# Optimization experiments

Measured on AMD Instinct MI355X. Metric: run time of the kernel, lower is better.

## Reference

```python
import jax, jax.numpy as jnp
import numpy as np

EPS = 1e-5
CLIP = 1.0

@jax.custom_vjp
def ste_sign(x):
    return jnp.sign(x)

def _ste_fwd(x):
    return jnp.sign(x), x

def _ste_bwd(x, g):
    return (g * (jnp.abs(x) <= CLIP).astype(g.dtype),)

ste_sign.defvjp(_ste_fwd, _ste_bwd)

def conv2d(x, w, stride, pad):
    return jax.lax.conv_general_dilated(
        x, w, window_strides=(stride, stride), padding=[(pad, pad), (pad, pad)],
        dimension_numbers=('NCHW', 'OIHW', 'NCHW'))

def bn(x, g, b, m, v):
    inv = g / jnp.sqrt(v + EPS)
    return x * inv[None, :, None, None] + (b - m * inv)[None, :, None, None]

def setup_inputs() -> dict:
    key = jax.random.key(0)
    ks = jax.random.split(key, 16)
    def rn(k, shape, scale=0.05):
        return jax.random.normal(k, shape, dtype=jnp.float32) * scale
    C = [64, 128, 128, 192, 192]
    d = {}
    d['x'] = jax.random.normal(ks[0], (128, 1, 128, 128), dtype=jnp.float32)
    d['conv1_w'] = rn(ks[1], (C[0], 1, 3, 3), 0.3)
    d['conv1_b'] = rn(ks[2], (C[0],))
    d['w2'] = rn(ks[3], (C[1], C[0], 3, 3), 0.3)
    d['w3'] = rn(ks[4], (C[2], C[1], 3, 3), 0.3)
    d['w4'] = rn(ks[5], (C[3], C[2], 3, 3), 0.3)
    d['w5'] = rn(ks[6], (C[4], C[3], 1, 1), 0.3)
    d['conv6_w'] = rn(ks[7], (12, C[4], 1, 1), 0.1)
    d['conv6_b'] = rn(ks[8], (12,))
    d['fc_w'] = rn(ks[9], (12, 12), 0.2)
    d['fc_b'] = rn(ks[10], (12,))
    for i, c in enumerate(C):
        kk = jax.random.split(jax.random.fold_in(key, 100 + i), 4)
        d[f'bn{i+1}_g'] = 1.0 + rn(kk[0], (c,), 0.1)
        d[f'bn{i+1}_b'] = rn(kk[1], (c,), 0.1)
        d[f'bn{i+1}_m'] = rn(kk[2], (c,), 0.1)
        d[f'bn{i+1}_v'] = 1.0 + jnp.abs(rn(kk[3], (c,), 0.1))
    return d

def reference(x, conv1_w, conv1_b, w2, w3, w4, w5, conv6_w, conv6_b, fc_w, fc_b,
              bn1_g, bn1_b, bn1_m, bn1_v, bn2_g, bn2_b, bn2_m, bn2_v,
              bn3_g, bn3_b, bn3_m, bn3_v, bn4_g, bn4_b, bn4_m, bn4_v,
              bn5_g, bn5_b, bn5_m, bn5_v):
    # conv1 (float) + BN + ReLU
    h = conv2d(x, conv1_w, 2, 1) + conv1_b[None, :, None, None]
    h = jax.nn.relu(bn(h, bn1_g, bn1_b, bn1_m, bn1_v))
    # binarized conv blocks: sign(activation) conv sign(weight)
    h = conv2d(ste_sign(h), ste_sign(w2), 1, 1)
    h = jax.nn.relu(bn(h, bn2_g, bn2_b, bn2_m, bn2_v))
    h = conv2d(ste_sign(h), ste_sign(w3), 2, 1)
    h = jax.nn.relu(bn(h, bn3_g, bn3_b, bn3_m, bn3_v))
    h = conv2d(ste_sign(h), ste_sign(w4), 1, 1)
    h = jax.nn.relu(bn(h, bn4_g, bn4_b, bn4_m, bn4_v))
    h = conv2d(ste_sign(h), ste_sign(w5), 1, 0)
    h = jax.nn.relu(bn(h, bn5_g, bn5_b, bn5_m, bn5_v))
    # 1x1 conv to classes, global average pool, FC, softmax
    h = conv2d(h, conv6_w, 1, 0) + conv6_b[None, :, None, None]
    h = jnp.mean(h, axis=(2, 3))  # [B, num_classes]
    logits = h @ fc_w.T + fc_b
    return jax.nn.softmax(logits, axis=1)
```

## Files before the change

kernel.cpp:

```cpp
#include <hip/hip_runtime.h>
#include <cstdint>

using u64 = unsigned long long;
using u32 = unsigned int;
typedef __attribute__((ext_vector_type(4))) int int4v;
typedef __attribute__((ext_vector_type(16))) int int16v;

struct PrepArgs {
  const float* bng[5]; const float* bnb[5]; const float* bnm[5]; const float* bnv[5];
  float* inv1; float* cc1; float* inv5; float* cc5;
  int* thr[3]; int* flp[3];
  const float* w[4];
  u64* wp[4]; u64* wz[4];
  u32* flags;
};

__global__ __launch_bounds__(256) void prep_all(PrepArgs a) {
  int i = blockIdx.x * 256 + threadIdx.x;
  if (i < 704) {
    const int off[6] = {0, 64, 192, 320, 512, 704};
    int l = 0;
    while (i >= off[l + 1]) ++l;
    int c = i - off[l];
    float iv = __fdiv_rn(a.bng[l][c], __fsqrt_rn(__fadd_rn(a.bnv[l][c], 1e-5f)));
    float cb = __fsub_rn(a.bnb[l][c], __fmul_rn(a.bnm[l][c], iv));
    if (l == 0) { a.inv1[c] = iv; a.cc1[c] = cb; }
    else if (l == 4) { a.inv5[c] = iv; a.cc5[c] = cb; }
    else {
      auto pred = [&](int v_) {
        return __fadd_rn(__fmul_rn((float)v_, iv), cb) > 0.f;
      };
      int Tx, fl;
      if (iv == 0.f) { Tx = pred(0) ? -100000 : 100000; fl = 0; }
      else if (iv > 0.f) {
        if (pred(-2048)) { Tx = -100000; fl = 0; }
        else if (!pred(2048)) { Tx = 100000; fl = 0; }
        else {
          int lo = -2048, hi = 2048;
          while (hi - lo > 1) { int md = (lo + hi) >> 1; if (pred(md)) hi = md; else lo = md; }
          Tx = hi; fl = 0;
        }
      } else {
        if (pred(2048)) { Tx = -100000; fl = -1; }
        else if (!pred(-2048)) { Tx = 100000; fl = -1; }
        else {
          int lo = -2048, hi = 2048;
          while (hi - lo > 1) { int md = (lo + hi) >> 1; if (pred(md)) lo = md; else hi = md; }
          Tx = lo ^ -1; fl = -1;
        }
      }
      a.thr[l - 1][c] = Tx; a.flp[l - 1][c] = fl;
    }
    return;
  }
  int j = i - 704;
  if (j >= 7488) return;
  const int poff[5] = {0, 1152, 3456, 6912, 7488};
  const int ICt[4] = {64, 128, 128, 192};
  const int Kt[4]  = {9, 9, 9, 1};
  const int Wt[4]  = {1, 2, 2, 3};
  int l = 0;
  while (j >= poff[l + 1]) ++l;
  int idx = j - poff[l];
  int W = Wt[l], K = Kt[l], IC = ICt[l];
  int wi = idx % W;
  int rest = idx / W;
  int t = rest % K;
  int oc = rest / K;
  u64 p = 0, z = 0;
  int icbase = wi * 64;
  int nb = IC - icbase; if (nb > 64) nb = 64;
  const float* w = a.w[l];
  for (int b = 0; b < nb; ++b) {
    float f = w[((size_t)oc * IC + (icbase + b)) * K + t];
    if (f > 0.f) p |= (1ull << b);
    else if (f == 0.f) z |= (1ull << b);
  }
  a.wp[l][idx] = p;
  a.wz[l][idx] = z;
  if (z) atomicOr(a.flags + l, 1u);
}

template <int CINW, int COUT>
__global__ __launch_bounds__(256) void prep_bfrag(const float* __restrict__ w,
                                                  signed char* __restrict__ bf) {
  constexpr int NKC = 9 * CINW;
  constexpr int NT = COUT / 16;
  constexpr int CIN = 64 * CINW;
  int idx = blockIdx.x * 256 + threadIdx.x;
  if (idx >= NT * NKC * 64) return;
  int lane = idx & 63;
  int rest = idx >> 6;
  int kc = rest % NKC;
  int t = rest / NKC;
  int tap = kc / CINW, wd = kc % CINW;
  int n = t * 16 + (lane & 15);
  int icb = wd * 64 + (lane >> 4) * 16;
  signed char* dst = bf + (size_t)idx * 16;
#pragma unroll
  for (int i = 0; i < 16; ++i) {
    float f = w[((size_t)n * CIN + icb + i) * 9 + tap];
    dst[i] = (f > 0.f) ? 1 : ((f < 0.f) ? -1 : 0);
  }
}

__global__ __launch_bounds__(256) void prep_bfrag32(const float* __restrict__ w,
                                                    signed char* __restrict__ bf) {
  int idx = blockIdx.x * 256 + threadIdx.x;
  if (idx >= 4 * 18 * 64) return;
  int lane = idx & 63;
  int rest = idx >> 6;
  int s = rest % 18;
  int t = rest / 18;
  int oc = t * 32 + (lane & 31);
  int kbase = s * 32 + (lane >> 5) * 16;
  signed char* dst = bf + (size_t)idx * 16;
#pragma unroll
  for (int i = 0; i < 16; ++i) {
    int k = kbase + i;
    int ch = k & 63, tap = k >> 6;
    float f = w[((size_t)oc * 64 + ch) * 9 + tap];
    dst[i] = (f > 0.f) ? 1 : ((f < 0.f) ? -1 : 0);
  }
}

__global__ __launch_bounds__(256) void pad_x(const float* __restrict__ x,
                                             float* __restrict__ xpad) {
  int idx = blockIdx.x * 256 + threadIdx.x;
  int c = idx & 127, r = (idx >> 7) & 127, n = idx >> 14;
  xpad[((size_t)n * 130 + r + 1) * 136 + c + 1] = x[idx];
}

__global__ __launch_bounds__(256) void conv1_bin(
    const float* __restrict__ xpad, const float* __restrict__ w1, const float* __restrict__ b1,
    const float* __restrict__ inv1, const float* __restrict__ cc1,
    u64* __restrict__ a1p) {
  int tid = threadIdx.x, lane = tid & 63;
  int rb = __builtin_amdgcn_readfirstlane(tid >> 6);
  int blk = blockIdx.x;
  int y = (blk % 16) * 4 + rb;
  int n = blk / 16;
  float W[9];
#pragma unroll
  for (int t = 0; t < 9; ++t) W[t] = w1[lane * 9 + t];
  float bias = b1[lane], iv = inv1[lane], cb = cc1[lane];
  const float* sb = xpad + ((size_t)n * 130 + 2 * y) * 136;
  float A[12], B[12], C[12];
  u64 rowm = 0;
  int xb = 0;

#define FLD(BUF, POFF)                                     \
  _Pragma("unroll") for (int _r = 0; _r < 3; ++_r)         \
  _Pragma("unroll") for (int _j = 0; _j < 4; ++_j)         \
    BUF[_r * 4 + _j] = sb[_r * 136 + (POFF) + _j];
#define FPX(XO, B0F, C0, B1F, C1, B2F, C2) {                          \
  float acc = 0.f;                                                    \
  _Pragma("unroll") for (int _r = 0; _r < 3; ++_r)                    \
    acc += B0F[_r * 4 + (C0)] * W[_r * 3 + 0]                         \
         + B1F[_r * 4 + (C1)] * W[_r * 3 + 1]                         \
         + B2F[_r * 4 + (C2)] * W[_r * 3 + 2];                        \
  float h = __fadd_rn(acc, bias);                                     \
  float bnv = __fadd_rn(__fmul_rn(h, iv), cb);                        \
  u64 _m = __ballot(bnv > 0.f);                                       \
  rowm = (lane == (XO)) ? _m : rowm; }
#define FSTEP(BA, BB, BC, POFF, XB)  \
  FLD(BC, (POFF) + 8);               \
  FPX((XB), BA, 0, BA, 1, BA, 2);    \
  FPX((XB) + 1, BA, 2, BA, 3, BB, 0);

  FLD(A, 0); FLD(B, 4);
  for (int g = 0; g < 10; ++g) {
    FSTEP(A, B, C, 0, xb);
    FSTEP(B, C, A, 4, xb + 2);
    FSTEP(C, A, B, 8, xb + 4);
    sb += 12; xb += 6;
  }
  FSTEP(A, B, C, 0, xb);
  FSTEP(B, C, A, 4, xb + 2);
  a1p[((size_t)n * 66 + (y + 1)) * 68 + lane + 1] = rowm;
#undef FLD
#undef FPX
#undef FSTEP
}

__global__ __launch_bounds__(256, 2) void bconv2_32(
    const u64* __restrict__ ain, const signed char* __restrict__ bf,
    const int* __restrict__ thr, const int* __restrict__ flp,
    u64* __restrict__ aout) {
  __shared__ int4v bs[4 * 18 * 64];
  int tid = threadIdx.x, lane = tid & 63;
  int wv = __builtin_amdgcn_readfirstlane(tid >> 6);
  int pos = blockIdx.x * 4 + wv;
  int xg = pos & 1;
  int y = (pos >> 1) & 63;
  int n = pos >> 7;
  int ln31 = lane & 31;
  int kg16 = (lane >> 5) * 16;
  int px = xg * 32 + ln31;

  const int4v* bfv = (const int4v*)bf;
  int4v breg[18];
#pragma unroll
  for (int i = 0; i < 18; ++i) breg[i] = bfv[tid + i * 256];

  const u64* abase = ain + ((size_t)n * 66 + y) * 68 + px;
  int4v af[18];
#pragma unroll
  for (int tap = 0; tap < 9; ++tap) {
    int dy = tap / 3, dx = tap % 3;
    u64 aw = abase[(size_t)dy * 68 + dx];
#pragma unroll
    for (int h = 0; h < 2; ++h) {
      u32 t16 = (u32)(aw >> (h * 32 + kg16)) & 0xFFFFu;
      int4v v;
      v.x = (int)((((t16      ) & 0xFu) * 0x00204081u) & 0x01010101u);
      v.y = (int)((((t16 >> 4 ) & 0xFu) * 0x00204081u) & 0x01010101u);
      v.z = (int)((((t16 >> 8 ) & 0xFu) * 0x00204081u) & 0x01010101u);
      v.w = (int)((((t16 >> 12) & 0xFu) * 0x00204081u) & 0x01010101u);
      af[tap * 2 + h] = v;
    }
  }

  int txv[4], flv[4];
#pragma unroll
  for (int t = 0; t < 4; ++t) { txv[t] = thr[t * 32 + ln31]; flv[t] = flp[t * 32 + ln31]; }

#pragma unroll
  for (int i = 0; i < 18; ++i) bs[tid + i * 256] = breg[i];
  __syncthreads();

  u32* out32 = (u32*)aout;
#pragma unroll
  for (int t = 0; t < 4; ++t) {
    int16v c = {0, 0, 0, 0, 0, 0, 0, 0, 0, 0, 0, 0, 0, 0, 0, 0};
#pragma unroll
    for (int s = 0; s < 18; ++s) {
      int4v bb = bs[(t * 18 + s) * 64 + lane];
      c = __builtin_amdgcn_mfma_i32_32x32x32_i8(af[s], bb, c, 0, 0, 0);
    }
    int tx = txv[t], fl = flv[t];
    u32 oww = 0;
#pragma unroll
    for (int r = 0; r < 16; ++r) {
      int plo = (r & 3) + 8 * (r >> 2);
      u64 bal = __ballot((c[r] ^ fl) >= tx);
      u32 wlo = (u32)bal, whi = (u32)(bal >> 32);
      oww = (lane == plo) ? wlo : oww;
      oww = (lane == plo + 4) ? whi : oww;
    }
    if (lane < 32) {
      int x = xg * 32 + lane;
      out32[(((size_t)n * 66 + (y + 1)) * 68 + (x + 1)) * 4 + t] = oww;
    }
  }
}

template <int CINW, int COUT, int STRIDE, int IN_HW, int OUT_HW, int MT, int TSTG, int OPAD>
__global__ __launch_bounds__(256) void bconv_mfma(
    const u64* __restrict__ ain, const signed char* __restrict__ bf,
    const int* __restrict__ thr, const int* __restrict__ flp,
    u64* __restrict__ aout) {
  constexpr int IPW = IN_HW + 4;
  constexpr int NKC = 9 * CINW;
  constexpr int NT = COUT / 16;
  constexpr int NSTG = NT / TSTG;
  constexpr int OCW = (COUT + 63) / 64;
  constexpr int XG = OUT_HW / (16 * MT);
  constexpr int FRAG = TSTG * NKC * 64;
  constexpr int CPT = (FRAG + 255) / 256;
  constexpr int NW32 = NT / 2;
  __shared__ int4v bs[FRAG];

  int tid = threadIdx.x, lane = tid & 63;
  int wv = __builtin_amdgcn_readfirstlane(tid >> 6);
  int pos = blockIdx.x * 4 + wv;
  int xg = pos % XG;
  int rest = pos / XG;
  int y = rest % OUT_HW;
  int n = rest / OUT_HW;
  int m = lane & 15;
  int kg = lane >> 4;

  const int4v* bfv = (const int4v*)bf;

  int4v breg[CPT];
#pragma unroll
  for (int i = 0; i < CPT; ++i) {
    int ix = tid + i * 256;
    if (FRAG % 256 == 0 || ix < FRAG) breg[i] = bfv[ix];
  }

  int4v af[MT * NKC];
#pragma unroll
  for (int mt = 0; mt < MT; ++mt) {
    int x = (xg * MT + mt) * 16 + m;
    const u64* abase = ain + (((size_t)n * (IN_HW + 2) + STRIDE * y) * IPW
                              + (size_t)STRIDE * x) * CINW;
#pragma unroll
    for (int dy = 0; dy < 3; ++dy)
#pragma unroll
      for (int dx = 0; dx < 3; ++dx)
#pragma unroll
        for (int wd = 0; wd < CINW; ++wd) {
          u64 aw = abase[((size_t)dy * IPW + dx) * CINW + wd];
          u32 t16 = (u32)(aw >> (kg * 16)) & 0xFFFFu;
          int4v v;
          v.x = (int)((((t16      ) & 0xFu) * 0x00204081u) & 0x01010101u);
          v.y = (int)((((t16 >> 4 ) & 0xFu) * 0x00204081u) & 0x01010101u);
          v.z = (int)((((t16 >> 8 ) & 0xFu) * 0x00204081u) & 0x01010101u);
          v.w = (int)((((t16 >> 12) & 0xFu) * 0x00204081u) & 0x01010101u);
          af[mt * NKC + (dy * 3 + dx) * CINW + wd] = v;
        }
  }

  u32 acc32[MT][NW32];
#pragma unroll
  for (int mt = 0; mt < MT; ++mt)
#pragma unroll
    for (int wl = 0; wl < NW32; ++wl) acc32[mt][wl] = 0;

#pragma unroll
  for (int s = 0; s < NSTG; ++s) {
    __syncthreads();
#pragma unroll
    for (int i = 0; i < CPT; ++i) {
      int ix = tid + i * 256;
      if (FRAG % 256 == 0 || ix < FRAG) bs[ix] = breg[i];
    }
    __syncthreads();
    if (s + 1 < NSTG) {
      const int4v* src = bfv + (size_t)(s + 1) * FRAG;
#pragma unroll
      for (int i = 0; i < CPT; ++i) {
        int ix = tid + i * 256;
        if (FRAG % 256 == 0 || ix < FRAG) breg[i] = src[ix];
      }
    }
#pragma unroll
    for (int tl = 0; tl < TSTG; ++tl) {
      int4v c[MT];
#pragma unroll
      for (int mt = 0; mt < MT; ++mt) c[mt] = (int4v){0, 0, 0, 0};
#pragma unroll
      for (int kc = 0; kc < NKC; ++kc) {
        int4v bb = bs[(tl * NKC + kc) * 64 + lane];
#pragma unroll
        for (int mt = 0; mt < MT; ++mt)
          c[mt] = __builtin_amdgcn_mfma_i32_16x16x64_i8(af[mt * NKC + kc], bb, c[mt], 0, 0, 0);
      }
      const int t = s * TSTG + tl;
      int tx = thr[t * 16 + m];
      int fl = flp[t * 16 + m];
#pragma unroll
      for (int mt = 0; mt < MT; ++mt) {
        u64 b0 = __ballot((c[mt].x ^ fl) >= tx);
        u64 b1 = __ballot((c[mt].y ^ fl) >= tx);
        u64 b2 = __ballot((c[mt].z ^ fl) >= tx);
        u64 b3 = __ballot((c[mt].w ^ fl) >= tx);
        u64 s01 = (m & 1) ? b1 : b0;
        u64 s23 = (m & 1) ? b3 : b2;
        u64 bsel = (m & 2) ? s23 : s01;
        u32 slice = (u32)(bsel >> ((m >> 2) * 16)) & 0xFFFFu;
        acc32[mt][t >> 1] |= slice << ((t & 1) * 16);
      }
    }
  }

  if (kg == 0) {
    u32* out32 = (u32*)aout;
#pragma unroll
    for (int mt = 0; mt < MT; ++mt) {
      int x = (xg * MT + mt) * 16 + m;
      size_t px32;
      if (OPAD)
        px32 = (((size_t)n * (OUT_HW + 2) + (y + 1)) * (OUT_HW + 4) + (x + 1)) * (OCW * 2);
      else
        px32 = (((size_t)n * OUT_HW + y) * OUT_HW + x) * (OCW * 2);
#pragma unroll
      for (int wl = 0; wl < NW32; ++wl)
        out32[px32 + wl] = acc32[mt][wl];
    }
  }
}

#define NCH5 8
__global__ __launch_bounds__(192) void bconv5_pool(
    const u64* __restrict__ ain, const u64* __restrict__ wp, const u64* __restrict__ wz,
    const u32* __restrict__ flag, const float* __restrict__ inv5, const float* __restrict__ cc5,
    float* __restrict__ partial) {
  int n = blockIdx.x / NCH5, ch = blockIdx.x % NCH5;
  int oc = threadIdx.x;
  u64 W0 = wp[oc * 3], W1 = wp[oc * 3 + 1], W2 = wp[oc * 3 + 2];
  bool anyz = (*flag != 0u);
  float iv = inv5[oc], cb = cc5[oc];
  const u64* sb = ain + ((size_t)n * 1024 + ch * 128) * 3;
  u64 A0, A1, A2, B0, B1, B2, C0, C1, C2;
  float acc = 0.f;
#define LD5(P, a0_, a1_, a2_) { a0_ = sb[(P) * 3]; a1_ = sb[(P) * 3 + 1]; a2_ = sb[(P) * 3 + 2]; }
#define PX5(a0_, a1_, a2_) {                                                   \
  int _pa = __popcll(a0_) + __popcll(a1_) + __popcll(a2_);                     \
  int _s = __popcll(a0_ & W0) + __popcll(a1_ & W1) + __popcll(a2_ & W2);       \
  int _val = 2 * _s - _pa;                                                     \
  if (anyz) _val += __popcll(a0_ & wz[oc * 3]) + __popcll(a1_ & wz[oc * 3 + 1])\
                  + __popcll(a2_ & wz[oc * 3 + 2]);                            \
  float _b = __fadd_rn(__fmul_rn((float)_val, iv), cb);                        \
  acc += fmaxf(_b, 0.f); }
  LD5(0, A0, A1, A2); LD5(1, B0, B1, B2);
  for (int g = 0; g < 42; ++g) {
    LD5(2, C0, C1, C2); PX5(A0, A1, A2);
    LD5(3, A0, A1, A2); PX5(B0, B1, B2);
    LD5(4, B0, B1, B2); PX5(C0, C1, C2);
    sb += 9;
  }
  PX5(A0, A1, A2); PX5(B0, B1, B2);
  partial[((size_t)n * NCH5 + ch) * 192 + oc] = acc;
#undef LD5
#undef PX5
}

__global__ __launch_bounds__(192) void head2(
    const float* __restrict__ partial,
    const float* __restrict__ w6, const float* __restrict__ b6,
    const float* __restrict__ fw, const float* __restrict__ fb,
    float* __restrict__ out) {
  __shared__ float pool_s[192];
  __shared__ float h6s[12];
  __shared__ float lgs[12];
  int n = blockIdx.x, t = threadIdx.x;
  float s = 0.f;
#pragma unroll
  for (int ch = 0; ch < NCH5; ++ch) s += partial[((size_t)n * NCH5 + ch) * 192 + t];
  pool_s[t] = s;
  __syncthreads();
  if (t < 12) {
    float a = 0.f;
    for (int c = 0; c < 192; ++c) a += pool_s[c] * w6[t * 192 + c];
    h6s[t] = b6[t] + a * (1.0f / 1024.0f);
  }
  __syncthreads();
  if (t < 12) {
    float s2 = fb[t];
    for (int k = 0; k < 12; ++k) s2 += h6s[k] * fw[t * 12 + k];
    lgs[t] = s2;
  }
  __syncthreads();
  if (t == 0) {
    float mx = -1e30f;
    for (int j = 0; j < 12; ++j) mx = fmaxf(mx, lgs[j]);
    float e[12], se = 0.f;
    for (int j = 0; j < 12; ++j) { e[j] = expf(lgs[j] - mx); se += e[j]; }
    for (int j = 0; j < 12; ++j) out[n * 12 + j] = e[j] / se;
  }
}

extern "C" void kernel_launch(void* const* d_in, const int* in_sizes, int n_in,
                              void* d_out, int out_size, void* d_ws, size_t ws_size,
                              hipStream_t stream) {
  const float* x   = (const float*)d_in[0];
  const float* w1  = (const float*)d_in[1];
  const float* b1  = (const float*)d_in[2];
  const float* w2  = (const float*)d_in[3];
  const float* w3  = (const float*)d_in[4];
  const float* w4  = (const float*)d_in[5];
  const float* w5  = (const float*)d_in[6];
  const float* w6  = (const float*)d_in[7];
  const float* b6  = (const float*)d_in[8];
  const float* fcw = (const float*)d_in[9];
  const float* fcb = (const float*)d_in[10];
  float* out = (float*)d_out;

  char* ws = (char*)d_ws;
  size_t off = 0;
  auto alloc = [&](size_t bytes) -> void* {
    void* p = ws + off;
    off += (bytes + 255) & ~(size_t)255;
    return p;
  };
  size_t xp_sz = (size_t)128 * 130 * 136 * 4;
  size_t a1_sz = (size_t)128 * 66 * 68 * 1 * 8;
  size_t a2_sz = (size_t)128 * 66 * 68 * 2 * 8;
  size_t a3_sz = (size_t)128 * 34 * 36 * 2 * 8;
  float* xpad = (float*)alloc(xp_sz);
  u64* a1p = (u64*)alloc(a1_sz);
  u64* a2p = (u64*)alloc(a2_sz);
  u64* a3p = (u64*)alloc(a3_sz);
  size_t zero_sz = xp_sz + a1_sz + a2_sz + a3_sz;
  u64* a4p = (u64*)alloc((size_t)128 * 32 * 32 * 3 * 8);
  float* partial = (float*)alloc((size_t)128 * NCH5 * 192 * 4);
  float* inv1 = (float*)alloc(64 * 4);
  float* cc1  = (float*)alloc(64 * 4);
  float* inv5 = (float*)alloc(192 * 4);
  float* cc5  = (float*)alloc(192 * 4);
  int* thr2 = (int*)alloc(128 * 4); int* flp2 = (int*)alloc(128 * 4);
  int* thr3 = (int*)alloc(128 * 4); int* flp3 = (int*)alloc(128 * 4);
  int* thr4 = (int*)alloc(192 * 4); int* flp4 = (int*)alloc(192 * 4);
  u64* wp2 = (u64*)alloc(128 * 9 * 1 * 8);
  u64* wz2 = (u64*)alloc(128 * 9 * 1 * 8);
  u64* wp3 = (u64*)alloc(128 * 9 * 2 * 8);
  u64* wz3 = (u64*)alloc(128 * 9 * 2 * 8);
  u64* wp4 = (u64*)alloc(192 * 9 * 2 * 8);
  u64* wz4 = (u64*)alloc(192 * 9 * 2 * 8);
  u64* wp5 = (u64*)alloc(192 * 1 * 3 * 8);
  u64* wz5 = (u64*)alloc(192 * 1 * 3 * 8);
  u32* flags = (u32*)alloc(4 * sizeof(u32));
  signed char* bf2x = (signed char*)alloc((size_t)4 * 18 * 64 * 16);
  signed char* bf3 = (signed char*)alloc((size_t)8 * 18 * 64 * 16);
  signed char* bf4 = (signed char*)alloc((size_t)12 * 18 * 64 * 16);
  (void)ws_size; (void)n_in; (void)in_sizes; (void)out_size;

  hipMemsetAsync(xpad, 0, zero_sz, stream);
  hipMemsetAsync(flags, 0, 4 * sizeof(u32), stream);

  PrepArgs pa;
  for (int l = 0; l < 5; ++l) {
    pa.bng[l] = (const float*)d_in[11 + 4 * l + 0];
    pa.bnb[l] = (const float*)d_in[11 + 4 * l + 1];
    pa.bnm[l] = (const float*)d_in[11 + 4 * l + 2];
    pa.bnv[l] = (const float*)d_in[11 + 4 * l + 3];
  }
  pa.inv1 = inv1; pa.cc1 = cc1; pa.inv5 = inv5; pa.cc5 = cc5;
  pa.thr[0] = thr2; pa.flp[0] = flp2;
  pa.thr[1] = thr3; pa.flp[1] = flp3;
  pa.thr[2] = thr4; pa.flp[2] = flp4;
  pa.w[0] = w2; pa.w[1] = w3; pa.w[2] = w4; pa.w[3] = w5;
  pa.wp[0] = wp2; pa.wp[1] = wp3; pa.wp[2] = wp4; pa.wp[3] = wp5;
  pa.wz[0] = wz2; pa.wz[1] = wz3; pa.wz[2] = wz4; pa.wz[3] = wz5;
  pa.flags = flags;
  prep_all<<<32, 256, 0, stream>>>(pa);

  prep_bfrag32<<<18, 256, 0, stream>>>(w2, bf2x);
  prep_bfrag<2, 128><<<(8 * 18 * 64 + 255) / 256, 256, 0, stream>>>(w3, bf3);
  prep_bfrag<2, 192><<<(12 * 18 * 64 + 255) / 256, 256, 0, stream>>>(w4, bf4);

  pad_x<<<(128 * 128 * 128) / 256, 256, 0, stream>>>(x, xpad);

  conv1_bin<<<128 * 16, 256, 0, stream>>>(xpad, w1, b1, inv1, cc1, a1p);

  bconv2_32<<<4096, 256, 0, stream>>>(a1p, bf2x, thr2, flp2, a2p);

  bconv_mfma<2, 128, 2, 64, 32, 1, 1, 1><<<2048, 256, 0, stream>>>(
      a2p, bf3, thr3, flp3, a3p);

  bconv_mfma<2, 192, 1, 32, 32, 1, 1, 0><<<2048, 256, 0, stream>>>(
      a3p, bf4, thr4, flp4, a4p);

  bconv5_pool<<<128 * NCH5, 192, 0, stream>>>(a4p, wp5, wz5, flags + 3, inv5, cc5, partial);

  head2<<<128, 192, 0, stream>>>(partial, w6, b6, fcw, fcb, out);
}
```

Before: 216.7 us.

## Fuse prep kernels into one launch and halve bconv2 shared-memory footprint

Five small prep/pad kernels are merged into a single 'front' kernel that dispatches on block index, removing several launch gaps. Separately, bconv2_32 now stages only half of the weight fragments in LDS at a time, loading the second half into registers while the first two output tiles are computed, and its launch bounds request 4 blocks per CU instead of 2. The aim is higher occupancy for the layer-2 conv and lower launch overhead, at the cost of extra barriers and a second LDS fill inside bconv2.

```diff
diff --git a/kernel.cpp b/kernel.cpp
--- a/kernel.cpp
+++ b/kernel.cpp
@@ -13,10 +13,11 @@
   const float* w[4];
   u64* wp[4]; u64* wz[4];
   u32* flags;
+  const float* x; float* xpad;
+  signed char* bf2x; signed char* bf3; signed char* bf4;
 };
 
-__global__ __launch_bounds__(256) void prep_all(PrepArgs a) {
-  int i = blockIdx.x * 256 + threadIdx.x;
+__device__ __forceinline__ void prep_all_body(const PrepArgs& a, int i) {
   if (i < 704) {
     const int off[6] = {0, 64, 192, 320, 512, 704};
     int l = 0;
@@ -82,12 +83,11 @@
 }
 
 template <int CINW, int COUT>
-__global__ __launch_bounds__(256) void prep_bfrag(const float* __restrict__ w,
-                                                  signed char* __restrict__ bf) {
+__device__ __forceinline__ void prep_bfrag_body(const float* __restrict__ w,
+                                                signed char* __restrict__ bf, int idx) {
   constexpr int NKC = 9 * CINW;
   constexpr int NT = COUT / 16;
   constexpr int CIN = 64 * CINW;
-  int idx = blockIdx.x * 256 + threadIdx.x;
   if (idx >= NT * NKC * 64) return;
   int lane = idx & 63;
   int rest = idx >> 6;
@@ -104,9 +104,8 @@
   }
 }
 
-__global__ __launch_bounds__(256) void prep_bfrag32(const float* __restrict__ w,
-                                                    signed char* __restrict__ bf) {
-  int idx = blockIdx.x * 256 + threadIdx.x;
+__device__ __forceinline__ void prep_bfrag32_body(const float* __restrict__ w,
+                                                  signed char* __restrict__ bf, int idx) {
   if (idx >= 4 * 18 * 64) return;
   int lane = idx & 63;
   int rest = idx >> 6;
@@ -124,11 +123,22 @@
   }
 }
 
-__global__ __launch_bounds__(256) void pad_x(const float* __restrict__ x,
-                                             float* __restrict__ xpad) {
-  int idx = blockIdx.x * 256 + threadIdx.x;
-  int c = idx & 127, r = (idx >> 7) & 127, n = idx >> 14;
-  xpad[((size_t)n * 130 + r + 1) * 136 + c + 1] = x[idx];
+__global__ __launch_bounds__(256) void front(PrepArgs a) {
+  int b = blockIdx.x, tid = threadIdx.x;
+  if (b < 8192) {
+    int idx = b * 256 + tid;
+    int c = idx & 127, r = (idx >> 7) & 127, n = idx >> 14;
+    a.xpad[((size_t)n * 130 + r + 1) * 136 + c + 1] = a.x[idx];
+    return;
+  }
+  b -= 8192;
+  if (b < 32) { prep_all_body(a, b * 256 + tid); return; }
+  b -= 32;
+  if (b < 18) { prep_bfrag32_body(a.w[0], a.bf2x, b * 256 + tid); return; }
+  b -= 18;
+  if (b < 36) { prep_bfrag_body<2, 128>(a.w[1], a.bf3, b * 256 + tid); return; }
+  b -= 36;
+  if (b < 54) { prep_bfrag_body<2, 192>(a.w[2], a.bf4, b * 256 + tid); return; }
 }
 
 __global__ __launch_bounds__(256) void conv1_bin(
@@ -183,11 +193,11 @@
 #undef FSTEP
 }
 
-__global__ __launch_bounds__(256, 2) void bconv2_32(
+__global__ __launch_bounds__(256, 4) void bconv2_32(
     const u64* __restrict__ ain, const signed char* __restrict__ bf,
     const int* __restrict__ thr, const int* __restrict__ flp,
     u64* __restrict__ aout) {
-  __shared__ int4v bs[4 * 18 * 64];
+  __shared__ int4v bs[2 * 18 * 64];
   int tid = threadIdx.x, lane = tid & 63;
   int wv = __builtin_amdgcn_readfirstlane(tid >> 6);
   int pos = blockIdx.x * 4 + wv;
@@ -199,9 +209,9 @@
   int px = xg * 32 + ln31;
 
   const int4v* bfv = (const int4v*)bf;
-  int4v breg[18];
-#pragma unroll
-  for (int i = 0; i < 18; ++i) breg[i] = bfv[tid + i * 256];
+  int4v breg[9];
+#pragma unroll
+  for (int i = 0; i < 9; ++i) breg[i] = bfv[tid + i * 256];
 
   const u64* abase = ain + ((size_t)n * 66 + y) * 68 + px;
   int4v af[18];
@@ -225,34 +235,55 @@
 #pragma unroll
   for (int t = 0; t < 4; ++t) { txv[t] = thr[t * 32 + ln31]; flv[t] = flp[t * 32 + ln31]; }
 
-#pragma unroll
-  for (int i = 0; i < 18; ++i) bs[tid + i * 256] = breg[i];
+  u32* out32 = (u32*)aout;
+
+#define C2_EPI(T, CREG) {                                             \
+  int tx = txv[T], fl = flv[T];                                       \
+  u32 oww = 0;                                                        \
+  _Pragma("unroll") for (int r = 0; r < 16; ++r) {                    \
+    int plo = (r & 3) + 8 * (r >> 2);                                 \
+    u64 bal = __ballot((CREG[r] ^ fl) >= tx);                         \
+    u32 wlo = (u32)bal, whi = (u32)(bal >> 32);                       \
+    oww = (lane == plo) ? wlo : oww;                                  \
+    oww = (lane == plo + 4) ? whi : oww;                              \
+  }                                                                   \
+  if (lane < 32) {                                                    \
+    int xx = xg * 32 + lane;                                          \
+    out32[(((size_t)n * 66 + (y + 1)) * 68 + (xx + 1)) * 4 + (T)] = oww; \
+  } }
+
+#pragma unroll
+  for (int i = 0; i < 9; ++i) bs[tid + i * 256] = breg[i];
   __syncthreads();
-
-  u32* out32 = (u32*)aout;
-#pragma unroll
-  for (int t = 0; t < 4; ++t) {
+#pragma unroll
+  for (int i = 0; i < 9; ++i) breg[i] = bfv[2 * 18 * 64 + tid + i * 256];
+
+#pragma unroll
+  for (int t = 0; t < 2; ++t) {
     int16v c = {0, 0, 0, 0, 0, 0, 0, 0, 0, 0, 0, 0, 0, 0, 0, 0};
 #pragma unroll
     for (int s = 0; s < 18; ++s) {
       int4v bb = bs[(t * 18 + s) * 64 + lane];
       c = __builtin_amdgcn_mfma_i32_32x32x32_i8(af[s], bb, c, 0, 0, 0);
     }
-    int tx = txv[t], fl = flv[t];
-    u32 oww = 0;
-#pragma unroll
-    for (int r = 0; r < 16; ++r) {
-      int plo = (r & 3) + 8 * (r >> 2);
-      u64 bal = __ballot((c[r] ^ fl) >= tx);
-      u32 wlo = (u32)bal, whi = (u32)(bal >> 32);
-      oww = (lane == plo) ? wlo : oww;
-      oww = (lane == plo + 4) ? whi : oww;
-    }
-    if (lane < 32) {
-      int x = xg * 32 + lane;
-      out32[(((size_t)n * 66 + (y + 1)) * 68 + (x + 1)) * 4 + t] = oww;
-    }
-  }
+    C2_EPI(t, c)
+  }
+
+  __syncthreads();
+#pragma unroll
+  for (int i = 0; i < 9; ++i) bs[tid + i * 256] = breg[i];
+  __syncthreads();
+#pragma unroll
+  for (int t = 2; t < 4; ++t) {
+    int16v c = {0, 0, 0, 0, 0, 0, 0, 0, 0, 0, 0, 0, 0, 0, 0, 0};
+#pragma unroll
+    for (int s = 0; s < 18; ++s) {
+      int4v bb = bs[((t - 2) * 18 + s) * 64 + lane];
+      c = __builtin_amdgcn_mfma_i32_32x32x32_i8(af[s], bb, c, 0, 0, 0);
+    }
+    C2_EPI(t, c)
+  }
+#undef C2_EPI
 }
 
 template <int CINW, int COUT, int STRIDE, int IN_HW, int OUT_HW, int MT, int TSTG, int OPAD>
@@ -526,13 +557,10 @@
   pa.wp[0] = wp2; pa.wp[1] = wp3; pa.wp[2] = wp4; pa.wp[3] = wp5;
   pa.wz[0] = wz2; pa.wz[1] = wz3; pa.wz[2] = wz4; pa.wz[3] = wz5;
   pa.flags = flags;
-  prep_all<<<32, 256, 0, stream>>>(pa);
-
-  prep_bfrag32<<<18, 256, 0, stream>>>(w2, bf2x);
-  prep_bfrag<2, 128><<<(8 * 18 * 64 + 255) / 256, 256, 0, stream>>>(w3, bf3);
-  prep_bfrag<2, 192><<<(12 * 18 * 64 + 255) / 256, 256, 0, stream>>>(w4, bf4);
-
-  pad_x<<<(128 * 128 * 128) / 256, 256, 0, stream>>>(x, xpad);
+  pa.x = x; pa.xpad = xpad;
+  pa.bf2x = bf2x; pa.bf3 = bf3; pa.bf4 = bf4;
+
+  front<<<8192 + 32 + 18 + 36 + 54, 256, 0, stream>>>(pa);
 
   conv1_bin<<<128 * 16, 256, 0, stream>>>(xpad, w1, b1, inv1, cc1, a1p);
 
```

After: 201.3 us. 7.1% less time.
